# Optimization experiments

Measured on AMD Instinct MI355X. Metric: run time of the kernel, lower is better.

Reference implementation:

```python
import jax, jax.numpy as jnp
import numpy as np

TAU = 1.0
EPS = 1e-10  # gumbel numerical floor


def rotation_6d_to_matrix(d6):
    # d6: [..., 6] -> [..., 3, 3] (rows b1,b2,b3), Gram-Schmidt (pytorch3d convention)
    a1, a2 = d6[..., :3], d6[..., 3:]
    b1 = a1 / jnp.linalg.norm(a1, axis=-1, keepdims=True)
    a2p = a2 - jnp.sum(b1 * a2, axis=-1, keepdims=True) * b1
    b2 = a2p / jnp.linalg.norm(a2p, axis=-1, keepdims=True)
    b3 = jnp.cross(b1, b2)
    return jnp.stack([b1, b2, b3], axis=-2)


def setup_inputs() -> dict:
    key = jax.random.key(0)
    ks = jax.random.split(key, 8)
    N, P, T = 65536, 16, 32
    cano_pc = jax.random.normal(ks[0], (N, 3), jnp.float32)
    w1 = jax.random.normal(ks[1], (128, 3), jnp.float32) * 0.3
    b1 = jnp.zeros((128,), jnp.float32)
    w2 = jax.random.normal(ks[2], (P, 128), jnp.float32) * 0.1
    b2 = jnp.zeros((P,), jnp.float32)
    proposal_6d = jnp.tile(jnp.array([1., 0., 0., 0., 1., 0.], jnp.float32), (T, P, 1)) \
        + 0.1 * jax.random.normal(ks[3], (T, P, 6), jnp.float32)
    proposal_t = 0.1 * jax.random.normal(ks[4], (T, P, 3), jnp.float32)
    # precomputed standard Gumbel noise for determinism
    u = jax.random.uniform(ks[5], (N, P), jnp.float32, minval=EPS, maxval=1.0 - EPS)
    gumbel = -jnp.log(-jnp.log(u))
    return {"cano_pc": cano_pc, "w1": w1, "b1": b1, "w2": w2, "b2": b2,
            "proposal_6d": proposal_6d, "proposal_t": proposal_t, "gumbel": gumbel}


def reference(cano_pc, w1, b1, w2, b2, proposal_6d, proposal_t, gumbel):
    T, P, _ = proposal_6d.shape
    N = cano_pc.shape[0]
    # seg_head: 1x1 Conv1d MLP 3 -> 128 -> P over N points
    h = jax.nn.relu(cano_pc @ w1.T + b1)           # [N,128]
    seg = h @ w2.T + b2                            # [N,P]
    # hard gumbel-softmax (straight-through); fwd value is exact one-hot
    y = jax.nn.softmax((seg + gumbel) / TAU, axis=-1)
    hard = jax.nn.one_hot(jnp.argmax(y, axis=-1), P, dtype=y.dtype)
    weight = hard + y - jax.lax.stop_gradient(y)   # [N,P]
    # per-(frame,part) rigid transforms
    R = rotation_6d_to_matrix(proposal_6d.reshape(-1, 6)).reshape(T, P, 3, 3)
    t = proposal_t                                 # [T,P,3]
    # dense apply: cano @ R^T + t for all (T,P)  -> [T,P,N,3]
    pc_trans = jnp.einsum('ni,tpji->tpnj', cano_pc, R) + t[:, :, None, :]
    # weighted combine over parts (weight is one-hot per point) -> [T,N,3]
    pc_out = jnp.einsum('np,tpnj->tnj', weight, pc_trans)
    # 4x4 transforms
    top = jnp.concatenate([R, t[..., None]], axis=-1)        # [T,P,3,4]
    bottom = jnp.broadcast_to(jnp.array([0., 0., 0., 1.], top.dtype), (T, P, 1, 4))
    trans_list = jnp.concatenate([top, bottom], axis=-2)     # [T,P,4,4]
    return pc_out, jnp.argmax(seg, axis=-1), trans_list
```

## Files before the change

### kernel.cpp

```cpp
#include <hip/hip_runtime.h>

#define N_PTS 65536
#define T_DIM 32
#define P_DIM 16

__global__ void prep_kernel(const float* __restrict__ d6,
                            const float* __restrict__ pt,
                            const float* __restrict__ w1,
                            const float* __restrict__ b1,
                            const float* __restrict__ w2,
                            const float* __restrict__ b2,
                            float* __restrict__ ws,
                            float* __restrict__ out_trans)
{
    int idx = blockIdx.x * blockDim.x + threadIdx.x;
    if (idx < T_DIM * P_DIM) {
        const float* a = d6 + idx * 6;
        float a1x=a[0], a1y=a[1], a1z=a[2], a2x=a[3], a2y=a[4], a2z=a[5];
        float n1 = sqrtf(a1x*a1x + a1y*a1y + a1z*a1z);
        float b1x=a1x/n1, b1y=a1y/n1, b1z=a1z/n1;
        float d = b1x*a2x + b1y*a2y + b1z*a2z;
        float px = a2x - d*b1x, py = a2y - d*b1y, pz = a2z - d*b1z;
        float n2 = sqrtf(px*px + py*py + pz*pz);
        float b2x=px/n2, b2y=py/n2, b2z=pz/n2;
        float b3x = b1y*b2z - b1z*b2y;
        float b3y = b1z*b2x - b1x*b2z;
        float b3z = b1x*b2y - b1y*b2x;
        float t0 = pt[idx*3+0], t1 = pt[idx*3+1], t2 = pt[idx*3+2];
        float* R = ws + idx*14;
        R[0]=b1x; R[1]=b1y; R[2]=b1z;
        R[3]=b2x; R[4]=b2y; R[5]=b2z;
        R[6]=b3x; R[7]=b3y; R[8]=b3z;
        R[9]=t0;  R[10]=t1; R[11]=t2;
        R[12]=0.f; R[13]=0.f;
        float* o = out_trans + idx*16;
        o[0]=b1x; o[1]=b1y; o[2]=b1z;  o[3]=t0;
        o[4]=b2x; o[5]=b2y; o[6]=b2z;  o[7]=t1;
        o[8]=b3x; o[9]=b3y; o[10]=b3z; o[11]=t2;
        o[12]=0.f; o[13]=0.f; o[14]=0.f; o[15]=1.f;
    }
    int k = idx - 512;
    if (k >= 0 && k < 128) {
        float* wp = ws + 7168 + k*20;
        wp[0]=w1[k*3+0]; wp[1]=w1[k*3+1]; wp[2]=w1[k*3+2]; wp[3]=b1[k];
        #pragma unroll
        for (int p=0;p<16;p++) wp[4+p] = w2[p*128+k];
    }
    if (idx < 16) ws[9728+idx] = b2[idx];
}

__global__ __launch_bounds__(256) void fused_kernel(
    const float* __restrict__ pc,
    const float* __restrict__ gumbel,
    const float* __restrict__ ws,
    float* __restrict__ out_pc,
    float* __restrict__ out_idx)
{
    __shared__ __align__(16) float smem[7168 + 64];
    const int tid  = threadIdx.x;
    const int lane = tid & 63;
    const int wv   = __builtin_amdgcn_readfirstlane(tid >> 6);
    const int n    = blockIdx.x * 64 + lane;

    const float x0 = pc[n*3+0], x1 = pc[n*3+1], x2 = pc[n*3+2];

    const float* wpk = ws + 7168 + wv*32*20;
    float seg[16];
    if (wv == 0) {
        const float* b2p = ws + 9728;
        #pragma unroll
        for (int p=0;p<16;p++) seg[p] = b2p[p];
    } else {
        #pragma unroll
        for (int p=0;p<16;p++) seg[p] = 0.f;
    }
    #pragma unroll 8
    for (int k=0;k<32;k++) {
        const float* wp = wpk + k*20;
        float h = fmaf(wp[0], x0, wp[3]);
        h = fmaf(wp[1], x1, h);
        h = fmaf(wp[2], x2, h);
        h = fmaxf(h, 0.0f);
        #pragma unroll
        for (int p=0;p<16;p++) seg[p] = fmaf(wp[4+p], h, seg[p]);
    }
    #pragma unroll
    for (int p=0;p<16;p++) smem[wv*1024 + p*64 + lane] = seg[p];
    __syncthreads();

    if (wv == 0) {
        float s[16];
        #pragma unroll
        for (int p=0;p<16;p++) {
            float v = smem[p*64 + lane] + smem[1024 + p*64 + lane];
            v += smem[2048 + p*64 + lane] + smem[3072 + p*64 + lane];
            s[p] = v;
        }
        float best = s[0]; int pseg = 0;
        #pragma unroll
        for (int p=1;p<16;p++) { if (s[p] > best) { best = s[p]; pseg = p; } }
        out_idx[n] = (float)pseg;

        float g[16];
        const float4* g4 = (const float4*)(gumbel + (size_t)n*16);
        #pragma unroll
        for (int j=0;j<4;j++) { float4 v = g4[j]; g[4*j]=v.x; g[4*j+1]=v.y; g[4*j+2]=v.z; g[4*j+3]=v.w; }
        float bg = s[0] + g[0]; int pstar = 0;
        #pragma unroll
        for (int p=1;p<16;p++) { float v = s[p] + g[p]; if (v > bg) { bg = v; pstar = p; } }
        smem[7168 + lane] = (float)pstar;
    }
    __syncthreads();

    {
        const float2* src = (const float2*)ws;
        float2* dst = (float2*)smem;
        #pragma unroll
        for (int i=0;i<14;i++) dst[tid + i*256] = src[tid + i*256];
    }
    __syncthreads();

    const int p = (int)smem[7168 + lane];
    const float* Rb = smem + p*14;
    #pragma unroll
    for (int i=0;i<8;i++) {
        const int t = wv*8 + i;
        const float* R = Rb + t*224;
        float2 r01 = *(const float2*)(R);
        float2 r23 = *(const float2*)(R+2);
        float2 r45 = *(const float2*)(R+4);
        float2 r67 = *(const float2*)(R+6);
        float2 r8t = *(const float2*)(R+8);
        float2 t12 = *(const float2*)(R+10);
        float y0 = fmaf(r01.x, x0, r8t.y); y0 = fmaf(r01.y, x1, y0); y0 = fmaf(r23.x, x2, y0);
        float y1 = fmaf(r23.y, x0, t12.x); y1 = fmaf(r45.x, x1, y1); y1 = fmaf(r45.y, x2, y1);
        float y2 = fmaf(r67.x, x0, t12.y); y2 = fmaf(r67.y, x1, y2); y2 = fmaf(r8t.x, x2, y2);
        float* o = out_pc + ((size_t)t * N_PTS + n) * 3;
        o[0]=y0; o[1]=y1; o[2]=y2;
    }
}

extern "C" void kernel_launch(void* const* d_in, const int* in_sizes, int n_in,
                              void* d_out, int out_size, void* d_ws, size_t ws_size,
                              hipStream_t stream)
{
    const float* pc  = (const float*)d_in[0];
    const float* w1  = (const float*)d_in[1];
    const float* b1  = (const float*)d_in[2];
    const float* w2  = (const float*)d_in[3];
    const float* b2  = (const float*)d_in[4];
    const float* d6  = (const float*)d_in[5];
    const float* pt  = (const float*)d_in[6];
    const float* gum = (const float*)d_in[7];
    float* out = (float*)d_out;
    float* ws  = (float*)d_ws;

    float* out_pc    = out;
    float* out_idx   = out + 6291456;
    float* out_trans = out + 6291456 + 65536;

    prep_kernel<<<3, 256, 0, stream>>>(d6, pt, w1, b1, w2, b2, ws, out_trans);
    fused_kernel<<<1024, 256, 0, stream>>>(pc, gum, ws, out_pc, out_idx);
}
```

Baseline: 87.66 us.

## Fold prep kernel into fused kernel and recompute rotations per block

Removes the separate prep kernel launch. Each block now builds all 512 rotation/translation entries in registers (two per thread) and writes them straight to shared memory; block 0 also writes the 4x4 transform output. The MLP reads w1/b1/w2 directly from global memory instead of the packed workspace, and the gumbel load is issued before the MLP loop so its latency is hidden. The intent is to drop a kernel launch and the workspace round-trip, at the cost of redundant Gram-Schmidt math in every block and less coalesced weight reads.

Result: slower. 89.61 us (+2.2%).

```diff
diff --git a/kernel.cpp b/kernel.cpp
--- a/kernel.cpp
+++ b/kernel.cpp
@@ -4,57 +4,18 @@
 #define T_DIM 32
 #define P_DIM 16
 
-__global__ void prep_kernel(const float* __restrict__ d6,
-                            const float* __restrict__ pt,
-                            const float* __restrict__ w1,
-                            const float* __restrict__ b1,
-                            const float* __restrict__ w2,
-                            const float* __restrict__ b2,
-                            float* __restrict__ ws,
-                            float* __restrict__ out_trans)
-{
-    int idx = blockIdx.x * blockDim.x + threadIdx.x;
-    if (idx < T_DIM * P_DIM) {
-        const float* a = d6 + idx * 6;
-        float a1x=a[0], a1y=a[1], a1z=a[2], a2x=a[3], a2y=a[4], a2z=a[5];
-        float n1 = sqrtf(a1x*a1x + a1y*a1y + a1z*a1z);
-        float b1x=a1x/n1, b1y=a1y/n1, b1z=a1z/n1;
-        float d = b1x*a2x + b1y*a2y + b1z*a2z;
-        float px = a2x - d*b1x, py = a2y - d*b1y, pz = a2z - d*b1z;
-        float n2 = sqrtf(px*px + py*py + pz*pz);
-        float b2x=px/n2, b2y=py/n2, b2z=pz/n2;
-        float b3x = b1y*b2z - b1z*b2y;
-        float b3y = b1z*b2x - b1x*b2z;
-        float b3z = b1x*b2y - b1y*b2x;
-        float t0 = pt[idx*3+0], t1 = pt[idx*3+1], t2 = pt[idx*3+2];
-        float* R = ws + idx*14;
-        R[0]=b1x; R[1]=b1y; R[2]=b1z;
-        R[3]=b2x; R[4]=b2y; R[5]=b2z;
-        R[6]=b3x; R[7]=b3y; R[8]=b3z;
-        R[9]=t0;  R[10]=t1; R[11]=t2;
-        R[12]=0.f; R[13]=0.f;
-        float* o = out_trans + idx*16;
-        o[0]=b1x; o[1]=b1y; o[2]=b1z;  o[3]=t0;
-        o[4]=b2x; o[5]=b2y; o[6]=b2z;  o[7]=t1;
-        o[8]=b3x; o[9]=b3y; o[10]=b3z; o[11]=t2;
-        o[12]=0.f; o[13]=0.f; o[14]=0.f; o[15]=1.f;
-    }
-    int k = idx - 512;
-    if (k >= 0 && k < 128) {
-        float* wp = ws + 7168 + k*20;
-        wp[0]=w1[k*3+0]; wp[1]=w1[k*3+1]; wp[2]=w1[k*3+2]; wp[3]=b1[k];
-        #pragma unroll
-        for (int p=0;p<16;p++) wp[4+p] = w2[p*128+k];
-    }
-    if (idx < 16) ws[9728+idx] = b2[idx];
-}
-
 __global__ __launch_bounds__(256) void fused_kernel(
     const float* __restrict__ pc,
+    const float* __restrict__ w1,
+    const float* __restrict__ b1,
+    const float* __restrict__ w2,
+    const float* __restrict__ b2,
+    const float* __restrict__ d6,
+    const float* __restrict__ pt,
     const float* __restrict__ gumbel,
-    const float* __restrict__ ws,
     float* __restrict__ out_pc,
-    float* __restrict__ out_idx)
+    float* __restrict__ out_idx,
+    float* __restrict__ out_trans)
 {
     __shared__ __align__(16) float smem[7168 + 64];
     const int tid  = threadIdx.x;
@@ -64,25 +25,61 @@
 
     const float x0 = pc[n*3+0], x1 = pc[n*3+1], x2 = pc[n*3+2];
 
-    const float* wpk = ws + 7168 + wv*32*20;
+    float Re[2][12];
+    #pragma unroll
+    for (int j=0;j<2;j++) {
+        const int e = tid + j*256;
+        const float* a = d6 + e*6;
+        float a1x=a[0], a1y=a[1], a1z=a[2], a2x=a[3], a2y=a[4], a2z=a[5];
+        float i1 = 1.0f / sqrtf(a1x*a1x + a1y*a1y + a1z*a1z);
+        float b1x=a1x*i1, b1y=a1y*i1, b1z=a1z*i1;
+        float d = b1x*a2x + b1y*a2y + b1z*a2z;
+        float px = a2x - d*b1x, py = a2y - d*b1y, pz = a2z - d*b1z;
+        float i2 = 1.0f / sqrtf(px*px + py*py + pz*pz);
+        float c0=px*i2, c1=py*i2, c2=pz*i2;
+        Re[j][0]=b1x; Re[j][1]=b1y; Re[j][2]=b1z;
+        Re[j][3]=c0;  Re[j][4]=c1;  Re[j][5]=c2;
+        Re[j][6]=b1y*c2 - b1z*c1;
+        Re[j][7]=b1z*c0 - b1x*c2;
+        Re[j][8]=b1x*c1 - b1y*c0;
+        Re[j][9]=pt[e*3+0]; Re[j][10]=pt[e*3+1]; Re[j][11]=pt[e*3+2];
+    }
+    if (blockIdx.x == 0) {
+        #pragma unroll
+        for (int j=0;j<2;j++) {
+            float* o = out_trans + (tid + j*256)*16;
+            o[0]=Re[j][0]; o[1]=Re[j][1]; o[2]=Re[j][2];  o[3]=Re[j][9];
+            o[4]=Re[j][3]; o[5]=Re[j][4]; o[6]=Re[j][5];  o[7]=Re[j][10];
+            o[8]=Re[j][6]; o[9]=Re[j][7]; o[10]=Re[j][8]; o[11]=Re[j][11];
+            o[12]=0.f; o[13]=0.f; o[14]=0.f; o[15]=1.f;
+        }
+    }
+
+    float g[16];
+    if (wv == 0) {
+        const float4* g4 = (const float4*)(gumbel + (size_t)n*16);
+        #pragma unroll
+        for (int j=0;j<4;j++) { float4 v = g4[j]; g[4*j]=v.x; g[4*j+1]=v.y; g[4*j+2]=v.z; g[4*j+3]=v.w; }
+    }
+
     float seg[16];
     if (wv == 0) {
-        const float* b2p = ws + 9728;
         #pragma unroll
-        for (int p=0;p<16;p++) seg[p] = b2p[p];
+        for (int p=0;p<16;p++) seg[p] = b2[p];
     } else {
         #pragma unroll
         for (int p=0;p<16;p++) seg[p] = 0.f;
     }
-    #pragma unroll 8
-    for (int k=0;k<32;k++) {
-        const float* wp = wpk + k*20;
-        float h = fmaf(wp[0], x0, wp[3]);
-        h = fmaf(wp[1], x1, h);
-        h = fmaf(wp[2], x2, h);
+    const int k0 = wv*32;
+    #pragma unroll 2
+    for (int kk=0;kk<32;kk++) {
+        const int k = k0 + kk;
+        float h = fmaf(w1[k*3+0], x0, b1[k]);
+        h = fmaf(w1[k*3+1], x1, h);
+        h = fmaf(w1[k*3+2], x2, h);
         h = fmaxf(h, 0.0f);
         #pragma unroll
-        for (int p=0;p<16;p++) seg[p] = fmaf(wp[4+p], h, seg[p]);
+        for (int p=0;p<16;p++) seg[p] = fmaf(w2[p*128+k], h, seg[p]);
     }
     #pragma unroll
     for (int p=0;p<16;p++) smem[wv*1024 + p*64 + lane] = seg[p];
@@ -100,11 +97,6 @@
         #pragma unroll
         for (int p=1;p<16;p++) { if (s[p] > best) { best = s[p]; pseg = p; } }
         out_idx[n] = (float)pseg;
-
-        float g[16];
-        const float4* g4 = (const float4*)(gumbel + (size_t)n*16);
-        #pragma unroll
-        for (int j=0;j<4;j++) { float4 v = g4[j]; g[4*j]=v.x; g[4*j+1]=v.y; g[4*j+2]=v.z; g[4*j+3]=v.w; }
         float bg = s[0] + g[0]; int pstar = 0;
         #pragma unroll
         for (int p=1;p<16;p++) { float v = s[p] + g[p]; if (v > bg) { bg = v; pstar = p; } }
@@ -112,15 +104,19 @@
     }
     __syncthreads();
 
-    {
-        const float2* src = (const float2*)ws;
-        float2* dst = (float2*)smem;
-        #pragma unroll
-        for (int i=0;i<14;i++) dst[tid + i*256] = src[tid + i*256];
+    #pragma unroll
+    for (int j=0;j<2;j++) {
+        float* R = smem + (tid + j*256)*14;
+        *(float2*)(R)    = make_float2(Re[j][0], Re[j][1]);
+        *(float2*)(R+2)  = make_float2(Re[j][2], Re[j][3]);
+        *(float2*)(R+4)  = make_float2(Re[j][4], Re[j][5]);
+        *(float2*)(R+6)  = make_float2(Re[j][6], Re[j][7]);
+        *(float2*)(R+8)  = make_float2(Re[j][8], Re[j][9]);
+        *(float2*)(R+10) = make_float2(Re[j][10], Re[j][11]);
     }
+    const int p = (int)smem[7168 + lane];
     __syncthreads();
 
-    const int p = (int)smem[7168 + lane];
     const float* Rb = smem + p*14;
     #pragma unroll
     for (int i=0;i<8;i++) {
@@ -153,12 +149,11 @@
     const float* pt  = (const float*)d_in[6];
     const float* gum = (const float*)d_in[7];
     float* out = (float*)d_out;
-    float* ws  = (float*)d_ws;
 
     float* out_pc    = out;
     float* out_idx   = out + 6291456;
     float* out_trans = out + 6291456 + 65536;
 
-    prep_kernel<<<3, 256, 0, stream>>>(d6, pt, w1, b1, w2, b2, ws, out_trans);
-    fused_kernel<<<1024, 256, 0, stream>>>(pc, gum, ws, out_pc, out_idx);
+    fused_kernel<<<1024, 256, 0, stream>>>(pc, w1, b1, w2, b2, d6, pt, gum,
+                                           out_pc, out_idx, out_trans);
 }
```
